# Optimization experiments

Measured on AMD Instinct MI355X. Metric: run time of the kernel, lower is better.

The kernel has to match this reference:

```python
import jax, jax.numpy as jnp
import numpy as np


def setup_inputs() -> dict:
    key = jax.random.key(0)
    k1, k2, k3, k4 = jax.random.split(key, 4)
    n_entity, n_rel, dim = 2048, 32, 512
    entities = jax.random.normal(k1, (n_entity, dim), dtype=jnp.float32)
    relations = jax.random.normal(k2, (n_rel, dim), dtype=jnp.float32)
    W = jax.random.normal(k3, (dim, dim), dtype=jnp.float32) * (1.0 / np.sqrt(dim))
    b = jax.random.normal(k4, (dim,), dtype=jnp.float32) * 0.01
    return {"entities": entities, "relations": relations, "W": W, "b": b}


def reference(entities, relations, W, b):
    # gate_nn applied to both entities and relations (shared Linear)
    E = entities @ W.T + b            # [n_entity, dim]
    R = relations @ W.T + b           # [n_rel, dim]
    # Diagonal RESCAL: scores[e, r, f] = sum_d E[e,d] * R[r,d] * E[f,d]
    # Equivalent to the per-relation loop E @ diag(R_r) @ E^T, fused into one einsum.
    scores = jnp.einsum('ed,rd,fd->erf', E, R, E)  # [n_entity, n_rel, n_entity]
    return scores
```

## Files before the change

kernel.cpp:

```cpp
#include <hip/hip_runtime.h>

typedef __attribute__((ext_vector_type(8))) __bf16 bf16x8;
typedef __attribute__((ext_vector_type(4))) float f32x4;

__device__ __forceinline__ float bf2f(unsigned int u) {
    return __uint_as_float(u << 16);
}
__device__ __forceinline__ unsigned short f2bf(float f) {
    unsigned int x = __float_as_uint(f);
    return (unsigned short)((x + 0x7fffu + ((x >> 16) & 1u)) >> 16);
}

__global__ void cast_all(const float* __restrict__ ent, const float* __restrict__ rel,
                         const float* __restrict__ W,
                         unsigned short* __restrict__ X_bf,
                         unsigned short* __restrict__ W_bf) {
    int i = blockIdx.x * blockDim.x + threadIdx.x;
    const float* src;
    unsigned short* dst;
    int g;
    if (i < 262144) {
        src = ent; dst = X_bf; g = i;
    } else if (i < 266240) {
        src = rel; dst = X_bf + 2048 * 512; g = i - 262144;
    } else {
        if (i >= 331776) return;
        src = W; dst = W_bf; g = i - 266240;
    }
    float4 v = reinterpret_cast<const float4*>(src)[g];
    ushort4 o;
    o.x = f2bf(v.x); o.y = f2bf(v.y); o.z = f2bf(v.z); o.w = f2bf(v.w);
    reinterpret_cast<ushort4*>(dst)[g] = o;
}

__device__ __forceinline__ unsigned int mul2bf(unsigned int a, unsigned int b) {
    float a0 = bf2f(a & 0xffffu), a1 = bf2f(a >> 16);
    float b0 = bf2f(b & 0xffffu), b1 = bf2f(b >> 16);
    return (unsigned int)f2bf(a0 * b0) | ((unsigned int)f2bf(a1 * b1) << 16);
}

__global__ void build_ap(const unsigned short* __restrict__ G,
                         unsigned short* __restrict__ Ap) {
    int t = blockIdx.x * blockDim.x + threadIdx.x;
    int row = t >> 6;
    int d = (t & 63) * 8;
    int e = row >> 5, r = row & 31;
    const uint4 ev = *reinterpret_cast<const uint4*>(G + e * 512 + d);
    const uint4 rv = *reinterpret_cast<const uint4*>(G + (2048 + r) * 512 + d);
    uint4 o;
    o.x = mul2bf(ev.x, rv.x);
    o.y = mul2bf(ev.y, rv.y);
    o.z = mul2bf(ev.z, rv.z);
    o.w = mul2bf(ev.w, rv.w);
    *reinterpret_cast<uint4*>(Ap + (size_t)row * 512 + d) = o;
}

#define BM 128
#define BN 128
#define BK 64

template <bool GUARD_M, bool BIAS_BF16OUT>
__global__ __launch_bounds__(256, 2) void mfma_gemm_bt(
    const unsigned short* __restrict__ A,
    const unsigned short* __restrict__ Bt,
    const float* __restrict__ bias,
    void* __restrict__ Cout,
    int M, int N, int K) {
    __shared__ __align__(16) unsigned short As[BM * BK];
    __shared__ __align__(16) unsigned short Bs[BN * BK];

    const int tid = threadIdx.x;
    const int lane = tid & 63;
    const int wave = tid >> 6;
    const int nbn = N / BN;
    const int bm0 = (blockIdx.x / nbn) * BM;
    const int bn0 = (blockIdx.x % nbn) * BN;
    const int wr = wave >> 1, wc = wave & 1;

    f32x4 acc[4][4] = {};

    const int srow = wave * 32 + (lane >> 3);
    const int scol = (lane & 7) * 8;

    for (int kb = 0; kb < K; kb += BK) {
#pragma unroll
        for (int i = 0; i < 4; ++i) {
            int row = bm0 + srow + i * 8;
            if (GUARD_M) row = min(row, M - 1);
            const unsigned short* src = A + (size_t)row * K + kb + scol;
            unsigned short* dst = &As[(wave * 32 + i * 8) * BK];
            __builtin_amdgcn_global_load_lds(
                (const __attribute__((address_space(1))) void*)src,
                (__attribute__((address_space(3))) void*)dst, 16, 0, 0);
        }
#pragma unroll
        for (int i = 0; i < 4; ++i) {
            int row = bn0 + srow + i * 8;
            const unsigned short* src = Bt + (size_t)row * K + kb + scol;
            unsigned short* dst = &Bs[(wave * 32 + i * 8) * BK];
            __builtin_amdgcn_global_load_lds(
                (const __attribute__((address_space(1))) void*)src,
                (__attribute__((address_space(3))) void*)dst, 16, 0, 0);
        }
        __syncthreads();

#pragma unroll
        for (int ks = 0; ks < BK / 32; ++ks) {
            const int k0 = ks * 32 + (lane >> 4) * 8;
            bf16x8 av[4], bv[4];
#pragma unroll
            for (int m = 0; m < 4; ++m)
                av[m] = *reinterpret_cast<const bf16x8*>(
                    &As[(wr * 64 + m * 16 + (lane & 15)) * BK + k0]);
#pragma unroll
            for (int n = 0; n < 4; ++n)
                bv[n] = *reinterpret_cast<const bf16x8*>(
                    &Bs[(wc * 64 + n * 16 + (lane & 15)) * BK + k0]);
#pragma unroll
            for (int m = 0; m < 4; ++m)
#pragma unroll
                for (int n = 0; n < 4; ++n)
                    acc[m][n] = __builtin_amdgcn_mfma_f32_16x16x32_bf16(
                        av[m], bv[n], acc[m][n], 0, 0, 0);
        }
        __syncthreads();
    }

#pragma unroll
    for (int m = 0; m < 4; ++m) {
#pragma unroll
        for (int n = 0; n < 4; ++n) {
#pragma unroll
            for (int j = 0; j < 4; ++j) {
                int row = bm0 + wr * 64 + m * 16 + (lane >> 4) * 4 + j;
                int col = bn0 + wc * 64 + n * 16 + (lane & 15);
                if (GUARD_M && row >= M) continue;
                float v = acc[m][n][j];
                if (BIAS_BF16OUT) {
                    v += bias[col];
                    ((unsigned short*)Cout)[(size_t)row * N + col] = f2bf(v);
                } else {
                    ((float*)Cout)[(size_t)row * N + col] = v;
                }
            }
        }
    }
}

#define NT8 8

__global__ __launch_bounds__(512, 2) void gemm256_8ph(
    const unsigned short* __restrict__ A,
    const unsigned short* __restrict__ B,
    float* __restrict__ C) {
    __shared__ __align__(16) unsigned short lds[65536];

    const int tid = threadIdx.x;
    const int lane = tid & 63;
    const int wave = tid >> 6;
    const int wr = wave >> 2;
    const int wc = wave & 3;
    const int laneM = lane & 15;
    const int laneK = (lane >> 4) * 8;
    const int kx = (lane & 7) * 8;

    const int swz = (blockIdx.x & 7) * 256 + (blockIdx.x >> 3);
    const int bm0 = (swz >> 3) * 256;
    const int bn0 = (swz & 7) * 256;

    const int sr0 = tid >> 3;
    const int sc = ((tid & 7) * 8) ^ (((tid >> 3) & 7) * 8);

    auto STAGE = [&](const unsigned short* mat, int row0, int kb, int slotOff) {
#pragma unroll
        for (int rd = 0; rd < 2; ++rd) {
            const unsigned short* src = mat + (size_t)(row0 + sr0 + rd * 64) * 512 + kb + sc;
            unsigned short* dst = &lds[slotOff + wave * 512 + rd * 4096];
            __builtin_amdgcn_global_load_lds(
                (const __attribute__((address_space(1))) void*)src,
                (__attribute__((address_space(3))) void*)dst, 16, 0, 0);
        }
    };
    auto RD = [&](int slotOff, int r, int ks) -> bf16x8 {
        return *reinterpret_cast<const bf16x8*>(
            &lds[slotOff + r * 64 + (((ks * 32) + laneK) ^ kx)]);
    };

    f32x4 acc[8][4] = {};
    bf16x8 av[4][2], bv0[2][2], bv1[2][2];

    STAGE(A, bm0,        0, 0 * 32768 + 0 * 8192);
    STAGE(B, bn0,        0, 0 * 32768 + 16384 + 0 * 8192);
    STAGE(B, bn0 + 128,  0, 0 * 32768 + 16384 + 1 * 8192);
    STAGE(A, bm0 + 128,  0, 0 * 32768 + 1 * 8192);
    STAGE(B, bn0,       64, 1 * 32768 + 16384 + 0 * 8192);
    STAGE(A, bm0,       64, 1 * 32768 + 0 * 8192);
    STAGE(B, bn0 + 128, 64, 1 * 32768 + 16384 + 1 * 8192);
    asm volatile("s_waitcnt vmcnt(6)" ::: "memory");
    __builtin_amdgcn_s_barrier();

#pragma unroll
    for (int t = 0; t < NT8; ++t) {
        const int P = t & 1;
        const int sA = P * 32768 + wr * 8192;
        const int sB = P * 32768 + 16384 + (wc >> 1) * 8192;
        const int rB = (wc & 1) * 64;

#pragma unroll
        for (int m = 0; m < 4; ++m)
#pragma unroll
            for (int ks = 0; ks < 2; ++ks)
                av[m][ks] = RD(sA, m * 16 + laneM, ks);
#pragma unroll
        for (int n = 0; n < 2; ++n)
#pragma unroll
            for (int ks = 0; ks < 2; ++ks)
                bv0[n][ks] = RD(sB, rB + n * 16 + laneM, ks);
        if (t + 1 < NT8)
            STAGE(A, bm0 + 128, (t + 1) * 64, ((t + 1) & 1) * 32768 + 8192);
        __builtin_amdgcn_s_barrier();
        asm volatile("s_waitcnt lgkmcnt(0)" ::: "memory");
        __builtin_amdgcn_sched_barrier(0);
        __builtin_amdgcn_s_setprio(1);
#pragma unroll
        for (int ks = 0; ks < 2; ++ks)
#pragma unroll
            for (int m = 0; m < 4; ++m)
#pragma unroll
                for (int n = 0; n < 2; ++n)
                    acc[m][n] = __builtin_amdgcn_mfma_f32_16x16x32_bf16(
                        bv0[n][ks], av[m][ks], acc[m][n], 0, 0, 0);
        __builtin_amdgcn_s_setprio(0);
        __builtin_amdgcn_s_barrier();

#pragma unroll
        for (int n = 0; n < 2; ++n)
#pragma unroll
            for (int ks = 0; ks < 2; ++ks)
                bv1[n][ks] = RD(sB, rB + (2 + n) * 16 + laneM, ks);
        __builtin_amdgcn_s_barrier();
        asm volatile("s_waitcnt lgkmcnt(0)" ::: "memory");
        __builtin_amdgcn_sched_barrier(0);
        __builtin_amdgcn_s_setprio(1);
#pragma unroll
        for (int ks = 0; ks < 2; ++ks)
#pragma unroll
            for (int m = 0; m < 4; ++m)
#pragma unroll
                for (int n = 0; n < 2; ++n)
                    acc[m][2 + n] = __builtin_amdgcn_mfma_f32_16x16x32_bf16(
                        bv1[n][ks], av[m][ks], acc[m][2 + n], 0, 0, 0);
        __builtin_amdgcn_s_setprio(0);
        __builtin_amdgcn_s_barrier();

#pragma unroll
        for (int m = 0; m < 4; ++m)
#pragma unroll
            for (int ks = 0; ks < 2; ++ks)
                av[m][ks] = RD(sA, 64 + m * 16 + laneM, ks);
        if (t + 2 < NT8)
            STAGE(B, bn0, (t + 2) * 64, ((t + 2) & 1) * 32768 + 16384);
        __builtin_amdgcn_s_barrier();
        asm volatile("s_waitcnt lgkmcnt(0)" ::: "memory");
        __builtin_amdgcn_sched_barrier(0);
        __builtin_amdgcn_s_setprio(1);
#pragma unroll
        for (int ks = 0; ks < 2; ++ks)
#pragma unroll
            for (int m = 0; m < 4; ++m)
#pragma unroll
                for (int n = 0; n < 2; ++n)
                    acc[4 + m][2 + n] = __builtin_amdgcn_mfma_f32_16x16x32_bf16(
                        bv1[n][ks], av[m][ks], acc[4 + m][2 + n], 0, 0, 0);
        __builtin_amdgcn_s_setprio(0);
        __builtin_amdgcn_s_barrier();

        if (t + 2 < NT8) {
            STAGE(A, bm0, (t + 2) * 64, ((t + 2) & 1) * 32768);
            STAGE(B, bn0 + 128, (t + 2) * 64, ((t + 2) & 1) * 32768 + 16384 + 8192);
        }
        __builtin_amdgcn_s_barrier();
        __builtin_amdgcn_s_setprio(1);
#pragma unroll
        for (int ks = 0; ks < 2; ++ks)
#pragma unroll
            for (int m = 0; m < 4; ++m)
#pragma unroll
                for (int n = 0; n < 2; ++n)
                    acc[4 + m][n] = __builtin_amdgcn_mfma_f32_16x16x32_bf16(
                        bv0[n][ks], av[m][ks], acc[4 + m][n], 0, 0, 0);
        __builtin_amdgcn_s_setprio(0);
        if (t < NT8 - 1) {
            if (t == NT8 - 2)
                asm volatile("s_waitcnt vmcnt(0)" ::: "memory");
            else
                asm volatile("s_waitcnt vmcnt(6)" ::: "memory");
            __builtin_amdgcn_s_barrier();
        }
    }

    {
        const int q = lane >> 4;
#pragma unroll
        for (int mi = 0; mi < 8; ++mi) {
            const int er = bm0 + wr * 128 + mi * 16 + laneM;
            float* dstRow = C + (size_t)er * 2048 + bn0 + wc * 64 + q * 4;
#pragma unroll
            for (int ni = 0; ni < 4; ++ni)
                __builtin_nontemporal_store(acc[mi][ni],
                                            (f32x4*)(dstRow + ni * 16));
        }
    }
}

extern "C" void kernel_launch(void* const* d_in, const int* in_sizes, int n_in,
                              void* d_out, int out_size, void* d_ws, size_t ws_size,
                              hipStream_t stream) {
    const float* entities  = (const float*)d_in[0];
    const float* relations = (const float*)d_in[1];
    const float* W         = (const float*)d_in[2];
    const float* b         = (const float*)d_in[3];

    char* ws = (char*)d_ws;
    unsigned short* W_bf = (unsigned short*)ws;
    unsigned short* X_bf = (unsigned short*)(ws + 524288);
    unsigned short* G_bf = (unsigned short*)(ws + 524288 + 2129920);
    unsigned short* Ap   = (unsigned short*)(ws + 524288 + 2129920 + 2129920);

    cast_all<<<1296, 256, 0, stream>>>(entities, relations, W, X_bf, W_bf);

    mfma_gemm_bt<true, true><<<17 * 4, 256, 0, stream>>>(
        X_bf, W_bf, b, (void*)G_bf, 2080, 512, 512);

    build_ap<<<16384, 256, 0, stream>>>(G_bf, Ap);

    gemm256_8ph<<<2048, 512, 0, stream>>>(Ap, G_bf, (float*)d_out);
}
```

Before: 243.2 us.

## Shrink main GEMM tile to 128x256 with triple-buffered K=32 stages and LDS epilogue

Replaces the 256x256 block tile with a 128x256 tile, a K step of 32 and a three-slot LDS ring, and raises launch bounds to allow four blocks per CU. The epilogue now stages accumulators through swizzled LDS so each row is written as contiguous 16-byte nontemporal stores. The aim is higher occupancy and better latency hiding, plus coalesced output writes for the large fp32 result. In exchange, A/B data reuse per block drops, so global/L2 traffic rises, and there are more barriers per unit of compute.

```diff
diff --git a/kernel.cpp b/kernel.cpp
--- a/kernel.cpp
+++ b/kernel.cpp
@@ -147,13 +147,13 @@
     }
 }
 
-#define NT8 8
-
-__global__ __launch_bounds__(512, 2) void gemm256_8ph(
+#define NT16 16
+
+__global__ __launch_bounds__(512, 4) void gemm128x256(
     const unsigned short* __restrict__ A,
     const unsigned short* __restrict__ B,
     float* __restrict__ C) {
-    __shared__ __align__(16) unsigned short lds[65536];
+    __shared__ __align__(16) unsigned short lds16[36864];
 
     const int tid = threadIdx.x;
     const int lane = tid & 63;
@@ -161,154 +161,125 @@
     const int wr = wave >> 2;
     const int wc = wave & 3;
     const int laneM = lane & 15;
-    const int laneK = (lane >> 4) * 8;
-    const int kx = (lane & 7) * 8;
-
-    const int swz = (blockIdx.x & 7) * 256 + (blockIdx.x >> 3);
-    const int bm0 = (swz >> 3) * 256;
+    const int q = lane >> 4;
+    const int laneK = q * 8;
+
+    const int swz = (blockIdx.x & 7) * 512 + (blockIdx.x >> 3);
+    const int bm0 = (swz >> 3) * 128;
     const int bn0 = (swz & 7) * 256;
 
-    const int sr0 = tid >> 3;
-    const int sc = ((tid & 7) * 8) ^ (((tid >> 3) & 7) * 8);
-
-    auto STAGE = [&](const unsigned short* mat, int row0, int kb, int slotOff) {
-#pragma unroll
-        for (int rd = 0; rd < 2; ++rd) {
-            const unsigned short* src = mat + (size_t)(row0 + sr0 + rd * 64) * 512 + kb + sc;
-            unsigned short* dst = &lds[slotOff + wave * 512 + rd * 4096];
-            __builtin_amdgcn_global_load_lds(
-                (const __attribute__((address_space(1))) void*)src,
-                (__attribute__((address_space(3))) void*)dst, 16, 0, 0);
-        }
+    const int sr = tid >> 2;
+    const int scs = ((tid & 3) * 8) ^ ((sr & 3) * 8);
+
+    auto STAGE = [&](const unsigned short* mat, int row0, int kb, int slotU) {
+        const unsigned short* src = mat + (size_t)(row0 + sr) * 512 + kb + scs;
+        __builtin_amdgcn_global_load_lds(
+            (const __attribute__((address_space(1))) void*)src,
+            (__attribute__((address_space(3))) void*)&lds16[slotU + wave * 512],
+            16, 0, 0);
     };
-    auto RD = [&](int slotOff, int r, int ks) -> bf16x8 {
+    auto RD = [&](int base, int rr) -> bf16x8 {
         return *reinterpret_cast<const bf16x8*>(
-            &lds[slotOff + r * 64 + (((ks * 32) + laneK) ^ kx)]);
+            &lds16[base + rr * 32 + (laneK ^ ((rr & 3) * 8))]);
     };
 
-    f32x4 acc[8][4] = {};
-    bf16x8 av[4][2], bv0[2][2], bv1[2][2];
-
-    STAGE(A, bm0,        0, 0 * 32768 + 0 * 8192);
-    STAGE(B, bn0,        0, 0 * 32768 + 16384 + 0 * 8192);
-    STAGE(B, bn0 + 128,  0, 0 * 32768 + 16384 + 1 * 8192);
-    STAGE(A, bm0 + 128,  0, 0 * 32768 + 1 * 8192);
-    STAGE(B, bn0,       64, 1 * 32768 + 16384 + 0 * 8192);
-    STAGE(A, bm0,       64, 1 * 32768 + 0 * 8192);
-    STAGE(B, bn0 + 128, 64, 1 * 32768 + 16384 + 1 * 8192);
-    asm volatile("s_waitcnt vmcnt(6)" ::: "memory");
+    f32x4 acc[4][4] = {};
+    bf16x8 av[4], bv0[2], bv1[2];
+
+    STAGE(A, bm0,        0, 0);
+    STAGE(B, bn0,        0, 4096);
+    STAGE(B, bn0 + 128,  0, 8192);
+    STAGE(A, bm0,       32, 12288);
+    STAGE(B, bn0,       32, 12288 + 4096);
+    STAGE(B, bn0 + 128, 32, 12288 + 8192);
+    asm volatile("s_waitcnt vmcnt(3)" ::: "memory");
     __builtin_amdgcn_s_barrier();
 
 #pragma unroll
-    for (int t = 0; t < NT8; ++t) {
-        const int P = t & 1;
-        const int sA = P * 32768 + wr * 8192;
-        const int sB = P * 32768 + 16384 + (wc >> 1) * 8192;
-        const int rB = (wc & 1) * 64;
+    for (int t = 0; t < NT16; ++t) {
+        const int base = (t % 3) * 12288;
+        const int nb = ((t + 2) % 3) * 12288;
 
 #pragma unroll
         for (int m = 0; m < 4; ++m)
-#pragma unroll
-            for (int ks = 0; ks < 2; ++ks)
-                av[m][ks] = RD(sA, m * 16 + laneM, ks);
+            av[m] = RD(base, wr * 64 + m * 16 + laneM);
 #pragma unroll
         for (int n = 0; n < 2; ++n)
-#pragma unroll
-            for (int ks = 0; ks < 2; ++ks)
-                bv0[n][ks] = RD(sB, rB + n * 16 + laneM, ks);
-        if (t + 1 < NT8)
-            STAGE(A, bm0 + 128, (t + 1) * 64, ((t + 1) & 1) * 32768 + 8192);
+            bv0[n] = RD(base + 4096, wc * 64 + n * 16 + laneM);
+        if (t + 2 < NT16) {
+            STAGE(A, bm0, (t + 2) * 32, nb);
+            STAGE(B, bn0, (t + 2) * 32, nb + 4096);
+        }
         __builtin_amdgcn_s_barrier();
         asm volatile("s_waitcnt lgkmcnt(0)" ::: "memory");
         __builtin_amdgcn_sched_barrier(0);
         __builtin_amdgcn_s_setprio(1);
 #pragma unroll
-        for (int ks = 0; ks < 2; ++ks)
-#pragma unroll
-            for (int m = 0; m < 4; ++m)
-#pragma unroll
-                for (int n = 0; n < 2; ++n)
-                    acc[m][n] = __builtin_amdgcn_mfma_f32_16x16x32_bf16(
-                        bv0[n][ks], av[m][ks], acc[m][n], 0, 0, 0);
+        for (int m = 0; m < 4; ++m)
+#pragma unroll
+            for (int n = 0; n < 2; ++n)
+                acc[m][n] = __builtin_amdgcn_mfma_f32_16x16x32_bf16(
+                    av[m], bv0[n], acc[m][n], 0, 0, 0);
         __builtin_amdgcn_s_setprio(0);
         __builtin_amdgcn_s_barrier();
 
 #pragma unroll
         for (int n = 0; n < 2; ++n)
-#pragma unroll
-            for (int ks = 0; ks < 2; ++ks)
-                bv1[n][ks] = RD(sB, rB + (2 + n) * 16 + laneM, ks);
+            bv1[n] = RD(base + 4096, wc * 64 + (2 + n) * 16 + laneM);
+        if (t + 2 < NT16)
+            STAGE(B, bn0 + 128, (t + 2) * 32, nb + 8192);
         __builtin_amdgcn_s_barrier();
         asm volatile("s_waitcnt lgkmcnt(0)" ::: "memory");
         __builtin_amdgcn_sched_barrier(0);
         __builtin_amdgcn_s_setprio(1);
 #pragma unroll
-        for (int ks = 0; ks < 2; ++ks)
-#pragma unroll
-            for (int m = 0; m < 4; ++m)
-#pragma unroll
-                for (int n = 0; n < 2; ++n)
-                    acc[m][2 + n] = __builtin_amdgcn_mfma_f32_16x16x32_bf16(
-                        bv1[n][ks], av[m][ks], acc[m][2 + n], 0, 0, 0);
+        for (int m = 0; m < 4; ++m)
+#pragma unroll
+            for (int n = 0; n < 2; ++n)
+                acc[m][2 + n] = __builtin_amdgcn_mfma_f32_16x16x32_bf16(
+                    av[m], bv1[n], acc[m][2 + n], 0, 0, 0);
         __builtin_amdgcn_s_setprio(0);
-        __builtin_amdgcn_s_barrier();
-
-#pragma unroll
-        for (int m = 0; m < 4; ++m)
-#pragma unroll
-            for (int ks = 0; ks < 2; ++ks)
-                av[m][ks] = RD(sA, 64 + m * 16 + laneM, ks);
-        if (t + 2 < NT8)
-            STAGE(B, bn0, (t + 2) * 64, ((t + 2) & 1) * 32768 + 16384);
-        __builtin_amdgcn_s_barrier();
-        asm volatile("s_waitcnt lgkmcnt(0)" ::: "memory");
-        __builtin_amdgcn_sched_barrier(0);
-        __builtin_amdgcn_s_setprio(1);
-#pragma unroll
-        for (int ks = 0; ks < 2; ++ks)
-#pragma unroll
-            for (int m = 0; m < 4; ++m)
-#pragma unroll
-                for (int n = 0; n < 2; ++n)
-                    acc[4 + m][2 + n] = __builtin_amdgcn_mfma_f32_16x16x32_bf16(
-                        bv1[n][ks], av[m][ks], acc[4 + m][2 + n], 0, 0, 0);
-        __builtin_amdgcn_s_setprio(0);
-        __builtin_amdgcn_s_barrier();
-
-        if (t + 2 < NT8) {
-            STAGE(A, bm0, (t + 2) * 64, ((t + 2) & 1) * 32768);
-            STAGE(B, bn0 + 128, (t + 2) * 64, ((t + 2) & 1) * 32768 + 16384 + 8192);
-        }
-        __builtin_amdgcn_s_barrier();
-        __builtin_amdgcn_s_setprio(1);
-#pragma unroll
-        for (int ks = 0; ks < 2; ++ks)
-#pragma unroll
-            for (int m = 0; m < 4; ++m)
-#pragma unroll
-                for (int n = 0; n < 2; ++n)
-                    acc[4 + m][n] = __builtin_amdgcn_mfma_f32_16x16x32_bf16(
-                        bv0[n][ks], av[m][ks], acc[4 + m][n], 0, 0, 0);
-        __builtin_amdgcn_s_setprio(0);
-        if (t < NT8 - 1) {
-            if (t == NT8 - 2)
+
+        if (t < NT16 - 1) {
+            if (t == NT16 - 2)
                 asm volatile("s_waitcnt vmcnt(0)" ::: "memory");
             else
-                asm volatile("s_waitcnt vmcnt(6)" ::: "memory");
+                asm volatile("s_waitcnt vmcnt(3)" ::: "memory");
             __builtin_amdgcn_s_barrier();
         }
     }
 
     {
-        const int q = lane >> 4;
-#pragma unroll
-        for (int mi = 0; mi < 8; ++mi) {
-            const int er = bm0 + wr * 128 + mi * 16 + laneM;
-            float* dstRow = C + (size_t)er * 2048 + bn0 + wc * 64 + q * 4;
-#pragma unroll
-            for (int ni = 0; ni < 4; ++ni)
-                __builtin_nontemporal_store(acc[mi][ni],
-                                            (f32x4*)(dstRow + ni * 16));
+        float* fb = (float*)lds16;
+#pragma unroll
+        for (int p = 0; p < 2; ++p) {
+            __syncthreads();
+            if (wr == p) {
+#pragma unroll
+                for (int m = 0; m < 4; ++m)
+#pragma unroll
+                    for (int n = 0; n < 4; ++n)
+#pragma unroll
+                        for (int j = 0; j < 4; ++j) {
+                            int L = m * 16 + q * 4 + j;
+                            int fl = wc * 64 + n * 16 + laneM;
+                            fb[L * 256 + (fl ^ ((L & 12) << 2))] = acc[m][n][j];
+                        }
+            }
+            __syncthreads();
+#pragma unroll
+            for (int rr = 0; rr < 2; ++rr) {
+                int R = wave * 8 + rr * 4 + q;
+                float* dstRow = C + (size_t)(bm0 + p * 64 + R) * 2048 + bn0;
+                int sx = (R & 12) << 2;
+#pragma unroll
+                for (int g = 0; g < 4; ++g) {
+                    int fl = g * 64 + laneM * 4;
+                    f32x4 v = *reinterpret_cast<const f32x4*>(
+                        &fb[R * 256 + (fl ^ sx)]);
+                    __builtin_nontemporal_store(v, (f32x4*)(dstRow + fl));
+                }
+            }
         }
     }
 }
@@ -334,5 +305,5 @@
 
     build_ap<<<16384, 256, 0, stream>>>(G_bf, Ap);
 
-    gemm256_8ph<<<2048, 512, 0, stream>>>(Ap, G_bf, (float*)d_out);
-}
+    gemm128x256<<<4096, 512, 0, stream>>>(Ap, G_bf, (float*)d_out);
+}
```

After: 203.6 us. 16.3% less time.
